# Performance work log

Measured on AMD Instinct MI355X. Metric: run time of the kernel, lower is better.

The kernel has to match this reference:

```python
import jax, jax.numpy as jnp
import numpy as np

MAXTIME = 1406073600
MINTIME = 832550400
SPAN = 10000
TIME_EMB = 100
N_GATE = 8
NUM_INTEREST = 4
DIM = 64
SEQ = 256
BATCH = 1024
ALPHA = 0.1
PI = 3.14159  # matches the literal in the source


def _build_time_table():
    # TimeEncoder: interleaved sin/cos positional table over time buckets.
    n = MAXTIME // SPAN + 3
    pos = np.arange(n, dtype=np.float64)[:, None]
    div = np.exp(np.arange(TIME_EMB // 2, dtype=np.float64) * -(np.log(10000.0) / TIME_EMB))[None, :]
    te = np.zeros((n, TIME_EMB), dtype=np.float32)
    te[:, 0::2] = np.sin(pos * div)
    te[:, 1::2] = np.cos(pos * div)
    return jnp.asarray(te)

_TIME_TABLE = _build_time_table()


def _time_encode(t):
    idx = (t / SPAN).astype(jnp.int32)
    return _TIME_TABLE[idx - jnp.min(idx)]


def setup_inputs() -> dict:
    key = jax.random.key(0)
    ks = jax.random.split(key, 11)
    B, S, D, NI, G = BATCH, SEQ, DIM, NUM_INTEREST, N_GATE
    item_his_emb = jax.random.normal(ks[0], (B, S, D), jnp.float32)
    item_eb = jax.random.normal(ks[1], (B, D), jnp.float32)
    # query times near maxtime, history times strictly earlier -> positive deltas
    t_batch = MAXTIME - 1e6 * jax.random.uniform(ks[2], (B,), jnp.float32)
    t_his = MINTIME + (MAXTIME - MINTIME - 1e6) * jax.random.uniform(ks[3], (B, S), jnp.float32)
    mask = (jax.random.uniform(ks[4], (B, S)) > 0.3).astype(jnp.float32)
    W1 = jax.random.normal(ks[5], (3 * TIME_EMB, 100), jnp.float32) / np.sqrt(3 * TIME_EMB)
    b1 = jnp.zeros((100,), jnp.float32)
    W2 = jax.random.normal(ks[6], (100, 1), jnp.float32) * 0.1
    b2 = jnp.zeros((1,), jnp.float32)
    phase = 100000.0 * jax.random.uniform(ks[7], (1, 1, G), jnp.float32)
    tao = 86400.0 * jnp.array([[[1, 2, 7, 14, 30, 60, 365, 730]]], jnp.float32)
    ratio = 0.3 * jax.random.uniform(ks[8], (1, 1, G), jnp.float32)
    gate_emb = jax.random.normal(ks[9], (1, D, G), jnp.float32)
    w_bilinear = jax.random.normal(ks[10], (S, NI * D, D), jnp.float32)
    return {"item_his_emb": item_his_emb, "item_eb": item_eb, "t_batch": t_batch,
            "t_his": t_his, "mask": mask, "W1": W1, "b1": b1, "W2": W2, "b2": b2,
            "phase": phase, "tao": tao, "ratio": ratio, "gate_emb": gate_emb,
            "w_bilinear": w_bilinear, "ta": 2}


def reference(item_his_emb, item_eb, t_batch, t_his, mask, W1, b1, W2, b2,
              phase, tao, ratio, gate_emb, w_bilinear, ta):
    B, S, D = item_his_emb.shape
    NI = NUM_INTEREST
    # --- time factor ---
    t_tiled = jnp.broadcast_to(t_batch[:, None], (B, S))
    time_feature = jnp.concatenate([_time_encode(t_tiled), _time_encode(t_his),
                                    _time_encode(t_tiled - t_his)], axis=2)  # [B,S,300]
    hidden1 = jax.nn.relu(time_feature @ W1 + b1)
    t_factor = jnp.transpose(jax.nn.sigmoid(hidden1 @ W2 + b2), (0, 2, 1))  # [B,1,S]
    # --- circadian gate factor ---
    phi = jnp.mod(t_his[:, :, None] - phase, tao) / tao  # [B,S,G]
    gate = jnp.where(phi < ratio, jnp.maximum(jnp.sin(PI * phi / ratio), 0.0), ALPHA * phi)
    gate_ratio = jax.nn.softmax(jnp.einsum('bsd,dg->bsg', item_his_emb, gate_emb[0]), axis=2) * gate
    g_factor = jnp.sum(gate_ratio, axis=2)[:, None, :]  # [B,1,S]
    reg1 = jnp.linalg.norm(t_factor)
    reg2 = jnp.linalg.norm(ratio) + jnp.linalg.norm(phase) / 100000.0
    # ta == 2 branch
    loss_reg = 0.1 * reg1 + 1.0 * reg2 + 1.0 / reg1 + 0.1 / reg2
    factor = jnp.broadcast_to(t_factor + g_factor, (B, NI, S))
    # --- bilinear_type == 2 projection ---
    item_emb_hat = jnp.einsum('skd,bsd->bsk', w_bilinear, item_his_emb)  # [B,S,NI*D]
    item_emb_hat = item_emb_hat.reshape(B, S, NI, D).transpose(0, 2, 1, 3)  # [B,NI,S,D]
    hat_iter = jax.lax.stop_gradient(item_emb_hat)
    # --- dynamic routing, 3 iterations ---
    cw = jnp.zeros((B, NI, S), item_his_emb.dtype)
    amask = mask[:, None, :]
    cap = None
    for i in range(3):
        sw = jax.nn.softmax(cw, axis=1)           # softmax over interests
        sw = jnp.where(amask == 0, 0.0, sw)
        src = hat_iter if i < 2 else item_emb_hat
        cap = jnp.einsum('bks,bksd->bkd', sw, src)  # [B,NI,D]
        n2 = jnp.sum(cap * cap, axis=-1, keepdims=True)
        cap = (n2 / (1.0 + n2) / jnp.sqrt(n2 + 1e-9)) * cap  # squash
        if i < 2:
            delta = jnp.einsum('bksd,bkd->bks', hat_iter, cap) * factor
            cw = cw + delta
    interest_capsule = cap  # [B,NI,D]
    # --- hard readout ---
    atten = jax.nn.softmax(jnp.einsum('bkd,bd->bk', interest_capsule, item_eb), axis=1)
    readout = interest_capsule[jnp.arange(B), jnp.argmax(atten, axis=1)]  # [B,D]
    return interest_capsule, readout, loss_reg
```

## Files before the change

kernel.cpp:

```cpp
#include <hip/hip_runtime.h>
#include <math.h>
#include <limits.h>

#define BB 1024
#define SS 256
#define DD 64
#define NI 4
#define NG 8
#define TE_N 100
#define PMAX 57420
#define ROWP 100
#define TPB 16

typedef _Float16 half8 __attribute__((ext_vector_type(8)));
typedef _Float16 half4 __attribute__((ext_vector_type(4)));
typedef float f32x4 __attribute__((ext_vector_type(4)));

#define OFF_FTH   ((size_t)0)
#define OFF_FDF   ((size_t)PMAX*ROWP)
#define OFF_GTB   ((size_t)2*PMAX*ROWP)
#define OFF_FAC   (OFF_GTB + (size_t)BB*ROWP)
#define OFF_SCAL  (OFF_FAC + (size_t)BB*SS)
#define OFF_REC   (OFF_SCAL + 160)
#define OFF_SREC  (OFF_REC + (size_t)BB*SS*2)
#define OFF_HAT   (OFF_SREC + (size_t)BB*SS*2)

__device__ inline float dpp_add_xor1(float x){
    int i = __builtin_bit_cast(int, x);
    int p = __builtin_amdgcn_update_dpp(i, i, 0xB1, 0xF, 0xF, true);
    return x + __builtin_bit_cast(float, p);
}
__device__ inline float dpp_add_xor2(float x){
    int i = __builtin_bit_cast(int, x);
    int p = __builtin_amdgcn_update_dpp(i, i, 0x4E, 0xF, 0xF, true);
    return x + __builtin_bit_cast(float, p);
}
__device__ inline float swz_add_xor16(float x){
    int i = __builtin_bit_cast(int, x);
    int p = __builtin_amdgcn_ds_swizzle(i, 0x401F);
    return x + __builtin_bit_cast(float, p);
}

__global__ void k_init(float* ws){
    int t = threadIdx.x;
    int* ib = (int*)(ws + OFF_SCAL);
    if (t == 0){
        ib[0] = INT_MAX; ib[1] = INT_MAX; ib[2] = INT_MAX;
        ws[OFF_SCAL + 4] = 0.0f;
    }
    if (t >= 8 && t < 136) ib[t] = 0;
}

__global__ void k_min(const float* __restrict__ tb, const float* __restrict__ th, float* ws){
    int gid = blockIdx.x * blockDim.x + threadIdx.x;
    int stride = gridDim.x * blockDim.x;
    int m0 = INT_MAX, m1 = INT_MAX, m2 = INT_MAX;
    for (int i = gid; i < BB*SS; i += stride){
        float t  = th[i];
        float t2 = tb[i >> 8];
        int i1 = (int)(t / 10000.0f);
        int i2 = (int)((t2 - t) / 10000.0f);
        m1 = min(m1, i1);
        m2 = min(m2, i2);
    }
    if (gid < BB) m0 = (int)(tb[gid] / 10000.0f);
    #pragma unroll
    for (int off = 1; off < 64; off <<= 1){
        m0 = min(m0, __shfl_xor(m0, off));
        m1 = min(m1, __shfl_xor(m1, off));
        m2 = min(m2, __shfl_xor(m2, off));
    }
    if ((threadIdx.x & 63) == 0){
        int* mi = (int*)(ws + OFF_SCAL);
        atomicMin(mi + 0, m0);
        atomicMin(mi + 1, m1);
        atomicMin(mi + 2, m2);
    }
}

__global__ void k_tables(const float* __restrict__ W1, float* ws){
    int pbase = blockIdx.x * TPB;
    int t = threadIdx.x;
    __shared__ float te[TPB][TE_N];
    for (int idx = t; idx < TPB*50; idx += 128){
        int pp = idx / 50, h = idx - pp*50;
        double div = exp((double)h * -0.09210340371976184);
        double a = (double)(pbase + pp) * div;
        te[pp][2*h]   = (float)sin(a);
        te[pp][2*h+1] = (float)cos(a);
    }
    __syncthreads();
    if (t < TE_N){
        float a1[TPB], a2[TPB];
        #pragma unroll
        for (int pp = 0; pp < TPB; pp++){ a1[pp] = 0.f; a2[pp] = 0.f; }
        for (int i = 0; i < TE_N; i++){
            float w1v = W1[(100+i)*100 + t];
            float w2v = W1[(200+i)*100 + t];
            #pragma unroll
            for (int pp = 0; pp < TPB; pp++){
                float v = te[pp][i];
                a1[pp] += v * w1v;
                a2[pp] += v * w2v;
            }
        }
        for (int pp = 0; pp < TPB; pp++){
            int p = pbase + pp;
            if (p < PMAX){
                ws[OFF_FTH + (size_t)p*ROWP + t] = a1[pp];
                ws[OFF_FDF + (size_t)p*ROWP + t] = a2[pp];
            }
        }
    }
}

__global__ void k_gtb(const float* __restrict__ tb, const float* __restrict__ W1,
                      const float* __restrict__ b1, float* ws){
    int b = blockIdx.x;
    int t = threadIdx.x;
    const int* mi = (const int*)(ws + OFF_SCAL);
    int p = (int)(tb[b] / 10000.0f) - mi[0];
    __shared__ float te[TE_N];
    if (t < TE_N/2){
        double div = exp((double)t * -0.09210340371976184);
        double a = (double)p * div;
        te[2*t]   = (float)sin(a);
        te[2*t+1] = (float)cos(a);
    }
    __syncthreads();
    if (t < TE_N){
        float a1 = b1[t];
        for (int i = 0; i < TE_N; i++) a1 += te[i] * W1[i*100 + t];
        ws[OFF_GTB + (size_t)b*ROWP + t] = a1;
    }
}

__global__ void __launch_bounds__(256) k_hist(const float* __restrict__ tb,
                                              const float* __restrict__ th, float* ws){
    __shared__ int lh[64];
    int t = threadIdx.x;
    if (t < 64) lh[t] = 0;
    __syncthreads();
    int gid = blockIdx.x*256 + t;
    int b = gid >> 8;
    const int* mi = (const int*)(ws + OFF_SCAL);
    float thv = th[gid], tbv = tb[b];
    int p1 = (int)(thv / 10000.0f) - mi[1];
    int p2 = (int)((tbv - thv) / 10000.0f) - mi[2];
    p1 = min(max(p1, 0), PMAX-1);
    p2 = min(max(p2, 0), PMAX-1);
    ((uint2*)(ws + OFF_REC))[gid] = make_uint2((unsigned)p1 | ((unsigned)p2 << 16), (unsigned)gid);
    atomicAdd(&lh[p1 >> 10], 1);
    __syncthreads();
    if (t < 64 && lh[t]) atomicAdd((int*)(ws + OFF_SCAL) + 8 + t, lh[t]);
}

__global__ void k_scan(float* ws){
    if (threadIdx.x == 0){
        int* g   = (int*)(ws + OFF_SCAL) + 8;
        int* cur = (int*)(ws + OFF_SCAL) + 72;
        int acc = 0;
        for (int i = 0; i < 64; i++){ cur[i] = acc; acc += g[i]; }
    }
}

__global__ void __launch_bounds__(256) k_scatter(float* ws){
    __shared__ int lh[64], lbase[64];
    int t = threadIdx.x;
    if (t < 64) lh[t] = 0;
    __syncthreads();
    int gid = blockIdx.x*256 + t;
    uint2 r = ((const uint2*)(ws + OFF_REC))[gid];
    int bkt = (int)(r.x & 0xFFFFu) >> 10;
    int myloc = atomicAdd(&lh[bkt], 1);
    __syncthreads();
    if (t < 64 && lh[t]) lbase[t] = atomicAdd((int*)(ws + OFF_SCAL) + 72 + t, lh[t]);
    __syncthreads();
    ((uint2*)(ws + OFF_SREC))[lbase[bkt] + myloc] = r;
}

__global__ void __launch_bounds__(256) k_factor2(const float* __restrict__ W2,
                         const float* __restrict__ b2, float* ws){
    int t = threadIdx.x;
    int lane = t & 63, wv = t >> 6;
    int bid = blockIdx.x;
    int sbid = (bid & 7)*256 + (bid >> 3);
    int pbase = sbid*128 + wv*32;

    bool tail = (lane < 36);
    float w2a = W2[lane];
    float w2b = tail ? W2[64 + lane] : 0.f;
    float bias = b2[0];

    unsigned rx = 0, ry = 0;
    if (lane < 32){
        uint2 r = ((const uint2*)(ws + OFF_SREC))[pbase + lane];
        rx = r.x; ry = r.y;
    }

    float tfkeep = 0.f, r1acc = 0.f;
    #pragma unroll 4
    for (int i = 0; i < 32; i++){
        unsigned rxi = (unsigned)__shfl((int)rx, i);
        unsigned ryi = (unsigned)__shfl((int)ry, i);
        int p1 = (int)(rxi & 0xFFFFu);
        int p2 = (int)(rxi >> 16);
        int bi = (int)(ryi >> 8);
        const float* r1 = ws + OFF_FTH + (size_t)p1*ROWP;
        const float* r2 = ws + OFF_FDF + (size_t)p2*ROWP;
        const float* rg = ws + OFF_GTB + (size_t)bi*ROWP;
        float a = r1[lane];
        float c = r2[lane];
        float g = rg[lane];
        float h = fmaxf(g + a + c, 0.f) * w2a;
        if (tail) h += fmaxf(rg[64+lane] + r1[64+lane] + r2[64+lane], 0.f) * w2b;
        h = dpp_add_xor1(h);
        h = dpp_add_xor2(h);
        h += __shfl_xor(h, 4);
        h += __shfl_xor(h, 8);
        h = swz_add_xor16(h);
        h += __shfl_xor(h, 32);
        float tf = 1.f / (1.f + expf(-(h + bias)));
        if (lane == i){ tfkeep = tf; r1acc = tf*tf; }
    }
    if (lane < 32) ws[OFF_FAC + ry] = tfkeep;
    #pragma unroll
    for (int off = 1; off < 64; off <<= 1) r1acc += __shfl_xor(r1acc, off);
    if (lane == 0) atomicAdd(ws + OFF_SCAL + 4, r1acc);
}

__global__ void __launch_bounds__(256) k_gate(const float* __restrict__ X,
      const float* __restrict__ th_, const float* __restrict__ phase,
      const float* __restrict__ tao, const float* __restrict__ ratio,
      const float* __restrict__ ge, float* ws){
    __shared__ float sge[NG][DD];
    int t = threadIdx.x;
    for (int i = t; i < DD*NG; i += 256) sge[i & 7][i >> 3] = ge[i];
    __syncthreads();
    int gid = blockIdx.x * 256 + t;

    float lg[NG];
    #pragma unroll
    for (int g = 0; g < NG; g++) lg[g] = 0.f;
    const float4* xr = (const float4*)(X + (size_t)gid*DD);
    #pragma unroll 4
    for (int dc = 0; dc < 16; dc++){
        float4 xv = xr[dc];
        #pragma unroll
        for (int g = 0; g < NG; g++){
            lg[g] += xv.x*sge[g][dc*4+0] + xv.y*sge[g][dc*4+1]
                   + xv.z*sge[g][dc*4+2] + xv.w*sge[g][dc*4+3];
        }
    }
    float mx = lg[0];
    #pragma unroll
    for (int g = 1; g < NG; g++) mx = fmaxf(mx, lg[g]);
    float thv = th_[gid];
    float es = 0.f, gf = 0.f;
    #pragma unroll
    for (int g = 0; g < NG; g++){
        float e = expf(lg[g] - mx);
        es += e;
        float phv = fmodf(thv - phase[g], tao[g]) / tao[g];
        float gv = (phv < ratio[g]) ? fmaxf(sinf(3.14159f*phv/ratio[g]), 0.f) : 0.1f*phv;
        gf += e * gv;
    }
    ws[OFF_FAC + gid] += gf / es;
}

__global__ void __launch_bounds__(512, 2)
k_hat(const float* __restrict__ X, const float* __restrict__ Wb,
      float* __restrict__ hat, int b0, int nb){
    int btile = blockIdx.x;
    int s     = blockIdx.y;
    int t     = threadIdx.x;
    int rows = nb - btile*64; if (rows > 64) rows = 64;

    __shared__ _Float16 lds[40960];

    const float* xbase = X + ((size_t)(b0 + btile*64)*SS + s)*DD;
    #pragma unroll
    for (int i = 0; i < 2; i++){
        int q = t + 512*i;
        int r = q >> 4, jf = q & 15;
        float4 v;
        if (r < rows) v = *(const float4*)(xbase + (size_t)r*SS*DD + jf*4);
        else { v.x = 0.f; v.y = 0.f; v.z = 0.f; v.w = 0.f; }
        half4 h, l;
        h.x = (_Float16)v.x; h.y = (_Float16)v.y; h.z = (_Float16)v.z; h.w = (_Float16)v.w;
        l.x = (_Float16)(v.x - (float)h.x); l.y = (_Float16)(v.y - (float)h.y);
        l.z = (_Float16)(v.z - (float)h.z); l.w = (_Float16)(v.w - (float)h.w);
        int bt = r >> 4, rowin = r & 15;
        int j0 = jf*4;
        int kk = j0 >> 5, jb = (j0 & 31) >> 3, e0 = j0 & 7;
        int lane = rowin + 16*jb;
        int base = ((bt*2 + kk)*2)*512 + lane*8 + e0;
        *(half4*)(lds + base)       = h;
        *(half4*)(lds + base + 512) = l;
    }
    const float* wbase = Wb + (size_t)s*16384;
    #pragma unroll
    for (int i = 0; i < 8; i++){
        int q = t + 512*i;
        int kd = q >> 4, jf = q & 15;
        float4 v = *(const float4*)(wbase + kd*64 + jf*4);
        half4 h, l;
        h.x = (_Float16)v.x; h.y = (_Float16)v.y; h.z = (_Float16)v.z; h.w = (_Float16)v.w;
        l.x = (_Float16)(v.x - (float)h.x); l.y = (_Float16)(v.y - (float)h.y);
        l.z = (_Float16)(v.z - (float)h.z); l.w = (_Float16)(v.w - (float)h.w);
        int kdt = kd >> 4, rowin = kd & 15;
        int j0 = jf*4;
        int kk = j0 >> 5, jb = (j0 & 31) >> 3, e0 = j0 & 7;
        int lane = rowin + 16*jb;
        int base = 8192 + ((kdt*2 + kk)*2)*512 + lane*8 + e0;
        *(half4*)(lds + base)       = h;
        *(half4*)(lds + base + 512) = l;
    }
    __syncthreads();

    int w    = t >> 6;
    int lane = t & 63;
    int wbt  = w >> 1;
    int kdh  = w & 1;

    half8 a[2][2];
    #pragma unroll
    for (int kk = 0; kk < 2; kk++)
        #pragma unroll
        for (int hl = 0; hl < 2; hl++)
            a[kk][hl] = *(half8*)(lds + ((wbt*2 + kk)*2 + hl)*512 + lane*8);

    int brow = (lane >> 4) * 4;
    int bcol = lane & 15;

    #pragma unroll
    for (int kdti = 0; kdti < 8; kdti++){
        int kdt = kdh*8 + kdti;
        const _Float16* wb0 = lds + 8192 + ((kdt*2 + 0)*2)*512 + lane*8;
        const _Float16* wb1 = lds + 8192 + ((kdt*2 + 1)*2)*512 + lane*8;
        half8 bh0 = *(half8*)(wb0);
        half8 bl0 = *(half8*)(wb0 + 512);
        half8 bh1 = *(half8*)(wb1);
        half8 bl1 = *(half8*)(wb1 + 512);
        f32x4 acc = {0.f, 0.f, 0.f, 0.f};
        acc = __builtin_amdgcn_mfma_f32_16x16x32_f16(a[0][0], bh0, acc, 0, 0, 0);
        acc = __builtin_amdgcn_mfma_f32_16x16x32_f16(a[0][0], bl0, acc, 0, 0, 0);
        acc = __builtin_amdgcn_mfma_f32_16x16x32_f16(a[0][1], bh0, acc, 0, 0, 0);
        acc = __builtin_amdgcn_mfma_f32_16x16x32_f16(a[1][0], bh1, acc, 0, 0, 0);
        acc = __builtin_amdgcn_mfma_f32_16x16x32_f16(a[1][0], bl1, acc, 0, 0, 0);
        acc = __builtin_amdgcn_mfma_f32_16x16x32_f16(a[1][1], bh1, acc, 0, 0, 0);
        int kd = kdt*16 + bcol;
        #pragma unroll
        for (int r = 0; r < 4; r++){
            int rl = wbt*16 + brow + r;
            if (rl < rows)
                hat[((size_t)(btile*64 + rl)*SS + s)*256 + kd] = acc[r];
        }
    }
}

__global__ void __launch_bounds__(1024) k_route(const float* __restrict__ eb,
                                                const float* __restrict__ mask_,
                                                const float* __restrict__ ws,
                                                const float* __restrict__ hat,
                                                float* __restrict__ out, int b0){
    int bl = blockIdx.x;
    int b = b0 + bl;
    int t = threadIdx.x;
    int lane = t & 63, wv = t >> 6;
    int k = (lane >> 2) & 3;
    int s_local = (lane & 3) | (((lane >> 4) & 3) << 2);
    int s = wv * 16 + s_local;
    __shared__ float part[16][4][64];
    __shared__ float capl[4][68];
    __shared__ float logits[4];
    __shared__ int kms;

    float hat_r[64];
    const float4* hsrc = (const float4*)(hat + (size_t)bl*65536 + ((size_t)s*4 + k)*64);
    #pragma unroll
    for (int jc = 0; jc < 16; jc++){
        float4 v = hsrc[jc];
        hat_r[4*jc] = v.x; hat_r[4*jc+1] = v.y; hat_r[4*jc+2] = v.z; hat_r[4*jc+3] = v.w;
    }
    float fac = ws[OFF_FAC + (size_t)b*SS + s];
    float mk = mask_[(size_t)b*SS + s];
    float cw = 0.f;
    float capv = 0.f;

    for (int it = 0; it < 3; ++it){
        float sw;
        if (it == 0){
            sw = (mk == 0.f) ? 0.f : 0.25f;
        } else {
            float m = fmaxf(cw, __shfl_xor(cw, 4)); m = fmaxf(m, __shfl_xor(m, 8));
            float e = expf(cw - m);
            float ssum = e + __shfl_xor(e, 4); ssum += __shfl_xor(ssum, 8);
            sw = (mk == 0.f) ? 0.f : (e / ssum);
        }

        #pragma unroll
        for (int c = 0; c < 4; c++){
            float tmp[16];
            #pragma unroll
            for (int i = 0; i < 16; i++) tmp[i] = sw * hat_r[c*16 + i];
            #pragma unroll
            for (int i = 0; i < 16; i++) tmp[i] = dpp_add_xor1(tmp[i]);
            #pragma unroll
            for (int i = 0; i < 16; i++) tmp[i] = dpp_add_xor2(tmp[i]);
            #pragma unroll
            for (int i = 0; i < 16; i++) tmp[i] = swz_add_xor16(tmp[i]);
            #pragma unroll
            for (int i = 0; i < 16; i++) tmp[i] += __shfl_xor(tmp[i], 32);
            if ((lane & 0x33) == 0){
                float* dst = &part[wv][lane >> 2][c*16];
                #pragma unroll
                for (int i = 0; i < 4; i++)
                    ((float4*)dst)[i] = make_float4(tmp[4*i], tmp[4*i+1], tmp[4*i+2], tmp[4*i+3]);
            }
        }
        __syncthreads();
        if (t < 256){
            int k2 = t >> 6, d = t & 63;
            float cp = 0.f;
            #pragma unroll
            for (int w2 = 0; w2 < 16; w2++) cp += part[w2][k2][d];
            float q = cp * cp;
            #pragma unroll
            for (int msk = 1; msk < 64; msk <<= 1) q += __shfl_xor(q, msk);
            float sc = q / ((1.f + q) * sqrtf(q + 1e-9f));
            capv = sc * cp;
            capl[k2][d] = capv;
        }
        __syncthreads();
        if (it < 2){
            const float4* cp4 = (const float4*)&capl[k][0];
            float dot = 0.f;
            #pragma unroll
            for (int jc = 0; jc < 16; jc++){
                float4 v = cp4[jc];
                dot += hat_r[4*jc]*v.x + hat_r[4*jc+1]*v.y + hat_r[4*jc+2]*v.z + hat_r[4*jc+3]*v.w;
            }
            cw += dot * fac;
        }
        __syncthreads();
    }

    if (t < 256){
        int k2 = t >> 6, d = t & 63;
        out[(size_t)b*256 + t] = capv;
        float qq = capv * eb[(size_t)b*DD + d];
        #pragma unroll
        for (int msk = 1; msk < 64; msk <<= 1) qq += __shfl_xor(qq, msk);
        if (lane == 0) logits[k2] = qq;
    }
    __syncthreads();
    if (t == 0){
        float best = logits[0]; int km = 0;
        for (int kk = 1; kk < 4; kk++) if (logits[kk] > best){ best = logits[kk]; km = kk; }
        kms = km;
    }
    __syncthreads();
    if (t < 64) out[(size_t)BB*256 + (size_t)b*64 + t] = capl[kms][t];
}

__global__ void k_final(const float* __restrict__ phase, const float* __restrict__ ratio,
                        float* ws, float* __restrict__ out){
    if (threadIdx.x == 0){
        float r2a = 0.f, r2b = 0.f;
        for (int g = 0; g < NG; g++){ r2a += ratio[g]*ratio[g]; r2b += phase[g]*phase[g]; }
        float reg2 = sqrtf(r2a) + sqrtf(r2b) / 100000.0f;
        float reg1 = sqrtf(ws[OFF_SCAL + 4]);
        out[(size_t)BB*256 + (size_t)BB*64] = 0.1f*reg1 + reg2 + 1.0f/reg1 + 0.1f/reg2;
    }
}

extern "C" void kernel_launch(void* const* d_in, const int* in_sizes, int n_in,
                              void* d_out, int out_size, void* d_ws, size_t ws_size,
                              hipStream_t stream){
    const float* Xh = (const float*)d_in[0];
    const float* eb = (const float*)d_in[1];
    const float* tb = (const float*)d_in[2];
    const float* th = (const float*)d_in[3];
    const float* mk = (const float*)d_in[4];
    const float* W1 = (const float*)d_in[5];
    const float* b1 = (const float*)d_in[6];
    const float* W2 = (const float*)d_in[7];
    const float* b2 = (const float*)d_in[8];
    const float* ph = (const float*)d_in[9];
    const float* ta = (const float*)d_in[10];
    const float* ra = (const float*)d_in[11];
    const float* ge = (const float*)d_in[12];
    const float* wb = (const float*)d_in[13];
    float* out = (float*)d_out;
    float* ws  = (float*)d_ws;

    hipLaunchKernelGGL(k_init,    dim3(1),    dim3(256), 0, stream, ws);
    hipLaunchKernelGGL(k_min,     dim3(256),  dim3(256), 0, stream, tb, th, ws);
    hipLaunchKernelGGL(k_tables,  dim3((PMAX+TPB-1)/TPB), dim3(128), 0, stream, W1, ws);
    hipLaunchKernelGGL(k_gtb,     dim3(BB),   dim3(128), 0, stream, tb, W1, b1, ws);
    hipLaunchKernelGGL(k_hist,    dim3(BB),   dim3(256), 0, stream, tb, th, ws);
    hipLaunchKernelGGL(k_scan,    dim3(1),    dim3(64),  0, stream, ws);
    hipLaunchKernelGGL(k_scatter, dim3(BB),   dim3(256), 0, stream, ws);
    hipLaunchKernelGGL(k_factor2, dim3(2*BB), dim3(256), 0, stream, W2, b2, ws);
    hipLaunchKernelGGL(k_gate,    dim3(BB),   dim3(256), 0, stream, Xh, th, ph, ta, ra, ge, ws);

    long wfloats  = (long)(ws_size / sizeof(float));
    long hatavail = wfloats - (long)OFF_HAT;
    int CH = (int)(hatavail / 65536);
    if (CH > BB) CH = BB;
    if (CH >= 128) CH &= ~127;
    if (CH < 1)  CH = 1;
    float* hatbuf = ws + OFF_HAT;
    for (int c0 = 0; c0 < BB; c0 += CH){
        int nb = BB - c0; if (nb > CH) nb = CH;
        int nbt = (nb + 63) / 64;
        hipLaunchKernelGGL(k_hat,   dim3(nbt, 256), dim3(512),  0, stream, Xh, wb, hatbuf, c0, nb);
        hipLaunchKernelGGL(k_route, dim3(nb),       dim3(1024), 0, stream, eb, mk, ws, hatbuf, out, c0);
    }
    hipLaunchKernelGGL(k_final, dim3(1), dim3(64), 0, stream, ph, ra, ws, out);
}
```

Before: 522.6 us.

## Transpose time-MLP tables and compute factor one element per thread

Stores the precomputed first-layer tables transposed (hidden unit major) so that threads holding sorted neighbouring bucket indices read adjacent addresses. The per-query bias table is now indexed by the quantized query-time bucket (at most 128 entries) rather than by batch row, and that bucket is packed into the record. k_factor2 changes from a wave-cooperative loop with cross-lane reductions per element to one thread per history element looping over the 100 hidden units. This removes the shuffle reductions and cuts the grid in half. The risk is that the p0 bucket count is assumed to stay below 128, and the gid field packed into 20 bits must fit.

```diff
diff --git a/kernel.cpp b/kernel.cpp
--- a/kernel.cpp
+++ b/kernel.cpp
@@ -9,17 +9,18 @@
 #define NG 8
 #define TE_N 100
 #define PMAX 57420
-#define ROWP 100
+#define PMAXP 57424
+#define P0MAX 128
 #define TPB 16
 
 typedef _Float16 half8 __attribute__((ext_vector_type(8)));
 typedef _Float16 half4 __attribute__((ext_vector_type(4)));
 typedef float f32x4 __attribute__((ext_vector_type(4)));
 
-#define OFF_FTH   ((size_t)0)
-#define OFF_FDF   ((size_t)PMAX*ROWP)
-#define OFF_GTB   ((size_t)2*PMAX*ROWP)
-#define OFF_FAC   (OFF_GTB + (size_t)BB*ROWP)
+#define OFF_FTHT  ((size_t)0)
+#define OFF_FDFT  ((size_t)TE_N*PMAXP)
+#define OFF_GTBP  (OFF_FDFT + (size_t)TE_N*PMAXP)
+#define OFF_FAC   (OFF_GTBP + (size_t)TE_N*P0MAX)
 #define OFF_SCAL  (OFF_FAC + (size_t)BB*SS)
 #define OFF_REC   (OFF_SCAL + 160)
 #define OFF_SREC  (OFF_REC + (size_t)BB*SS*2)
@@ -107,23 +108,20 @@
         for (int pp = 0; pp < TPB; pp++){
             int p = pbase + pp;
             if (p < PMAX){
-                ws[OFF_FTH + (size_t)p*ROWP + t] = a1[pp];
-                ws[OFF_FDF + (size_t)p*ROWP + t] = a2[pp];
+                ws[OFF_FTHT + (size_t)t*PMAXP + p] = a1[pp];
+                ws[OFF_FDFT + (size_t)t*PMAXP + p] = a2[pp];
             }
         }
     }
 }
 
-__global__ void k_gtb(const float* __restrict__ tb, const float* __restrict__ W1,
-                      const float* __restrict__ b1, float* ws){
-    int b = blockIdx.x;
-    int t = threadIdx.x;
-    const int* mi = (const int*)(ws + OFF_SCAL);
-    int p = (int)(tb[b] / 10000.0f) - mi[0];
+__global__ void k_gtbP(const float* __restrict__ W1, const float* __restrict__ b1, float* ws){
+    int p0 = blockIdx.x;
+    int t = threadIdx.x;
     __shared__ float te[TE_N];
     if (t < TE_N/2){
         double div = exp((double)t * -0.09210340371976184);
-        double a = (double)p * div;
+        double a = (double)p0 * div;
         te[2*t]   = (float)sin(a);
         te[2*t+1] = (float)cos(a);
     }
@@ -131,7 +129,7 @@
     if (t < TE_N){
         float a1 = b1[t];
         for (int i = 0; i < TE_N; i++) a1 += te[i] * W1[i*100 + t];
-        ws[OFF_GTB + (size_t)b*ROWP + t] = a1;
+        ws[OFF_GTBP + (size_t)t*P0MAX + p0] = a1;
     }
 }
 
@@ -147,9 +145,12 @@
     float thv = th[gid], tbv = tb[b];
     int p1 = (int)(thv / 10000.0f) - mi[1];
     int p2 = (int)((tbv - thv) / 10000.0f) - mi[2];
+    int p0 = (int)(tbv / 10000.0f) - mi[0];
     p1 = min(max(p1, 0), PMAX-1);
     p2 = min(max(p2, 0), PMAX-1);
-    ((uint2*)(ws + OFF_REC))[gid] = make_uint2((unsigned)p1 | ((unsigned)p2 << 16), (unsigned)gid);
+    p0 = min(max(p0, 0), P0MAX-1);
+    ((uint2*)(ws + OFF_REC))[gid] =
+        make_uint2((unsigned)p1 | ((unsigned)p2 << 16), (unsigned)gid | ((unsigned)p0 << 20));
     atomicAdd(&lh[p1 >> 10], 1);
     __syncthreads();
     if (t < 64 && lh[t]) atomicAdd((int*)(ws + OFF_SCAL) + 8 + t, lh[t]);
@@ -182,51 +183,34 @@
 __global__ void __launch_bounds__(256) k_factor2(const float* __restrict__ W2,
                          const float* __restrict__ b2, float* ws){
     int t = threadIdx.x;
-    int lane = t & 63, wv = t >> 6;
     int bid = blockIdx.x;
-    int sbid = (bid & 7)*256 + (bid >> 3);
-    int pbase = sbid*128 + wv*32;
-
-    bool tail = (lane < 36);
-    float w2a = W2[lane];
-    float w2b = tail ? W2[64 + lane] : 0.f;
-    float bias = b2[0];
-
-    unsigned rx = 0, ry = 0;
-    if (lane < 32){
-        uint2 r = ((const uint2*)(ws + OFF_SREC))[pbase + lane];
-        rx = r.x; ry = r.y;
-    }
-
-    float tfkeep = 0.f, r1acc = 0.f;
-    #pragma unroll 4
-    for (int i = 0; i < 32; i++){
-        unsigned rxi = (unsigned)__shfl((int)rx, i);
-        unsigned ryi = (unsigned)__shfl((int)ry, i);
-        int p1 = (int)(rxi & 0xFFFFu);
-        int p2 = (int)(rxi >> 16);
-        int bi = (int)(ryi >> 8);
-        const float* r1 = ws + OFF_FTH + (size_t)p1*ROWP;
-        const float* r2 = ws + OFF_FDF + (size_t)p2*ROWP;
-        const float* rg = ws + OFF_GTB + (size_t)bi*ROWP;
-        float a = r1[lane];
-        float c = r2[lane];
-        float g = rg[lane];
-        float h = fmaxf(g + a + c, 0.f) * w2a;
-        if (tail) h += fmaxf(rg[64+lane] + r1[64+lane] + r2[64+lane], 0.f) * w2b;
-        h = dpp_add_xor1(h);
-        h = dpp_add_xor2(h);
-        h += __shfl_xor(h, 4);
-        h += __shfl_xor(h, 8);
-        h = swz_add_xor16(h);
-        h += __shfl_xor(h, 32);
-        float tf = 1.f / (1.f + expf(-(h + bias)));
-        if (lane == i){ tfkeep = tf; r1acc = tf*tf; }
-    }
-    if (lane < 32) ws[OFF_FAC + ry] = tfkeep;
-    #pragma unroll
-    for (int off = 1; off < 64; off <<= 1) r1acc += __shfl_xor(r1acc, off);
-    if (lane == 0) atomicAdd(ws + OFF_SCAL + 4, r1acc);
+    int sbid = (bid & 7)*128 + (bid >> 3);
+    int q = sbid*256 + t;
+    uint2 r = ((const uint2*)(ws + OFF_SREC))[q];
+    int p1  = (int)(r.x & 0xFFFFu);
+    int p2  = (int)(r.x >> 16);
+    int gid = (int)(r.y & 0xFFFFFu);
+    int p0  = (int)(r.y >> 20);
+
+    const float* ft = ws + OFF_FTHT + p1;
+    const float* fd = ws + OFF_FDFT + p2;
+    const float* gp = ws + OFF_GTBP + p0;
+
+    float z = 0.f;
+    #pragma unroll 10
+    for (int j = 0; j < TE_N; j++){
+        float a = ft[(size_t)j*PMAXP];
+        float c = fd[(size_t)j*PMAXP];
+        float g = gp[(size_t)j*P0MAX];
+        z += fmaxf(g + a + c, 0.f) * W2[j];
+    }
+    float tf = 1.f / (1.f + expf(-(z + b2[0])));
+    ws[OFF_FAC + gid] = tf;
+
+    float r1 = tf * tf;
+    #pragma unroll
+    for (int off = 1; off < 64; off <<= 1) r1 += __shfl_xor(r1, off);
+    if ((t & 63) == 0) atomicAdd(ws + OFF_SCAL + 4, r1);
 }
 
 __global__ void __launch_bounds__(256) k_gate(const float* __restrict__ X,
@@ -495,15 +479,15 @@
     float* out = (float*)d_out;
     float* ws  = (float*)d_ws;
 
-    hipLaunchKernelGGL(k_init,    dim3(1),    dim3(256), 0, stream, ws);
-    hipLaunchKernelGGL(k_min,     dim3(256),  dim3(256), 0, stream, tb, th, ws);
+    hipLaunchKernelGGL(k_init,    dim3(1),     dim3(256), 0, stream, ws);
+    hipLaunchKernelGGL(k_min,     dim3(256),   dim3(256), 0, stream, tb, th, ws);
     hipLaunchKernelGGL(k_tables,  dim3((PMAX+TPB-1)/TPB), dim3(128), 0, stream, W1, ws);
-    hipLaunchKernelGGL(k_gtb,     dim3(BB),   dim3(128), 0, stream, tb, W1, b1, ws);
-    hipLaunchKernelGGL(k_hist,    dim3(BB),   dim3(256), 0, stream, tb, th, ws);
-    hipLaunchKernelGGL(k_scan,    dim3(1),    dim3(64),  0, stream, ws);
-    hipLaunchKernelGGL(k_scatter, dim3(BB),   dim3(256), 0, stream, ws);
-    hipLaunchKernelGGL(k_factor2, dim3(2*BB), dim3(256), 0, stream, W2, b2, ws);
-    hipLaunchKernelGGL(k_gate,    dim3(BB),   dim3(256), 0, stream, Xh, th, ph, ta, ra, ge, ws);
+    hipLaunchKernelGGL(k_gtbP,    dim3(P0MAX), dim3(128), 0, stream, W1, b1, ws);
+    hipLaunchKernelGGL(k_hist,    dim3(BB),    dim3(256), 0, stream, tb, th, ws);
+    hipLaunchKernelGGL(k_scan,    dim3(1),     dim3(64),  0, stream, ws);
+    hipLaunchKernelGGL(k_scatter, dim3(BB),    dim3(256), 0, stream, ws);
+    hipLaunchKernelGGL(k_factor2, dim3(BB),    dim3(256), 0, stream, W2, b2, ws);
+    hipLaunchKernelGGL(k_gate,    dim3(BB),    dim3(256), 0, stream, Xh, th, ph, ta, ra, ge, ws);
 
     long wfloats  = (long)(ws_size / sizeof(float));
     long hatavail = wfloats - (long)OFF_HAT;
```

New measurement: 525.4 us. About the same (+0.5%).
